# Performance work log

Measured on AMD Instinct MI355X. Metric: run time of the kernel, lower is better.

Reference implementation:

```python
import jax, jax.numpy as jnp
import numpy as np

D_MODEL = 1024
D_INNER = 2048   # expand=2
D_STATE = 16
D_CONV = 4
DT_RANK = 64     # ceil(d_model/16)
B_SZ = 2
L_SEQ = 2048
EPS = 1e-6


def setup_inputs() -> dict:
    key = jax.random.key(0)
    ks = jax.random.split(key, 9)
    def g(k, shape, scale=0.02):
        return jax.random.normal(k, shape, jnp.float32) * scale
    return {
        "x": jax.random.normal(ks[0], (B_SZ, L_SEQ, D_MODEL), jnp.float32),
        "ln_gamma": jnp.ones((D_MODEL,), jnp.float32),
        "ln_beta": jnp.zeros((D_MODEL,), jnp.float32),
        "in_proj_w": g(ks[1], (2 * D_INNER, D_MODEL)),
        "conv_w": g(ks[2], (D_INNER, 1, D_CONV), 0.1),
        "conv_b": g(ks[3], (D_INNER,), 0.1),
        "x_proj_w": g(ks[4], (DT_RANK + 2 * D_STATE, D_INNER)),
        "dt_proj_w": g(ks[5], (D_INNER, DT_RANK), 0.1),
        "dt_proj_b": g(ks[6], (D_INNER,), 0.1),
        "A_log": jnp.log(jnp.broadcast_to(jnp.arange(1, D_STATE + 1, dtype=jnp.float32), (D_INNER, D_STATE))),
        "D": jnp.ones((D_INNER,), jnp.float32),
        "out_proj_w": g(ks[7], (D_MODEL, D_INNER)),
    }


def _silu(v):
    return v * jax.nn.sigmoid(v)


def reference(x, ln_gamma, ln_beta, in_proj_w, conv_w, conv_b, x_proj_w,
              dt_proj_w, dt_proj_b, A_log, D, out_proj_w):
    B, L, _ = x.shape
    # LayerNorm (eps=1e-6)
    mu = x.mean(-1, keepdims=True)
    var = x.var(-1, keepdims=True)
    h = (x - mu) / jnp.sqrt(var + EPS) * ln_gamma + ln_beta
    # in_proj -> (B, 2*d_inner, L)
    xz = jnp.einsum('bld,ed->bel', h, in_proj_w)
    u, z = jnp.split(xz, 2, axis=1)
    # depthwise causal conv1d (padding=d_conv-1, then [..., :L]) + SiLU
    up = jnp.pad(u, ((0, 0), (0, 0), (D_CONV - 1, 0)))
    uc = jax.lax.conv_general_dilated(
        up, conv_w, (1,), 'VALID',
        dimension_numbers=('NCH', 'OIH', 'NCH'),
        feature_group_count=D_INNER)
    uc = _silu(uc + conv_b[None, :, None])  # (B, d_inner, L)
    # x_proj -> dt, B, C
    x_dbl = jnp.einsum('bdl,ed->ble', uc, x_proj_w)
    dt, Bm, Cm = jnp.split(x_dbl, [DT_RANK, DT_RANK + D_STATE], axis=-1)
    delta = jnp.einsum('blr,dr->bdl', dt, dt_proj_w) + dt_proj_b[None, :, None]
    delta = jax.nn.softplus(delta)  # delta_softplus=True with dt_proj bias
    A = -jnp.exp(A_log)  # (d_inner, d_state)
    deltaA = jnp.exp(jnp.einsum('bdl,dn->bdln', delta, A))
    Bm = jnp.transpose(Bm, (0, 2, 1))  # (B, n, L)
    Cm = jnp.transpose(Cm, (0, 2, 1))  # (B, n, L)
    deltaB_u = jnp.einsum('bdl,bnl,bdl->bdln', delta, Bm, uc)

    def step(state, inp):
        dA, dBu, Ct = inp  # (B,d,n), (B,d,n), (B,n)
        state = dA * state + dBu
        y = jnp.einsum('bdn,bn->bd', state, Ct)
        return state, y

    init = jnp.zeros((B, D_INNER, D_STATE), jnp.float32)
    _, ys = jax.lax.scan(
        step, init,
        (jnp.moveaxis(deltaA, 2, 0), jnp.moveaxis(deltaB_u, 2, 0), jnp.moveaxis(Cm, 2, 0)))
    y = jnp.moveaxis(ys, 0, 2)  # (B, d_inner, L)
    y = y + uc * D[None, :, None]
    y = y * _silu(z)
    out = jnp.einsum('bdl,ed->ble', y, out_proj_w)
    return out + x  # residual
```

## Files before the change

kernel.cpp:

```cpp
#include <hip/hip_runtime.h>
#include <hip/hip_bf16.h>

#define D_MODEL 1024
#define D_INNER 2048
#define D_STATE 16
#define D_CONV  4
#define DT_RANK 64
#define B_SZ    2
#define L_SEQ   2048
#define NTOK    (B_SZ * L_SEQ)
#define XD      (DT_RANK + 2 * D_STATE)
#define NCHUNK  64
#define TC      (L_SEQ / NCHUNK)
#define SPLITK  8

#define WS_U     0
#define WS_Z     16777216
#define WS_UC    33554432
#define WS_DY    50331648
#define WS_XDBL  67108864
#define WS_FLAG  67895296
#define WS_NEED  67895552
#define WS_W     67895552
#define OFF_INW  0
#define OFF_OUTW 8388608
#define OFF_XW   12582912
#define OFF_DTW  12976128
#define WS_FULL  81133824

typedef __attribute__((ext_vector_type(8))) short short8;
typedef __attribute__((ext_vector_type(4))) float float4v;

#define GAS __attribute__((address_space(1)))
#define LAS __attribute__((address_space(3)))
__device__ __forceinline__ void gload_lds16(const ushort* g, ushort* l) {
    __builtin_amdgcn_global_load_lds((const GAS uint*)g, (LAS uint*)l, 16, 0, 0);
}

__device__ __forceinline__ float bf2f_u(ushort u) {
    union { uint i; float f; } c; c.i = ((uint)u) << 16; return c.f;
}
__device__ __forceinline__ float u2f(uint u) {
    union { uint i; float f; } c; c.i = u; return c.f;
}
__device__ __forceinline__ ushort f2bf_u(float f) {
    union { float f; uint i; } c; c.f = f;
    uint r = c.i + 0x7FFFu + ((c.i >> 16) & 1u);
    return (ushort)(r >> 16);
}
__device__ __forceinline__ float silu_f(float v) {
    return v * __builtin_amdgcn_rcpf(1.f + __expf(-v));
}
__device__ __forceinline__ float softplus_f(float v) {
    return (v > 15.f) ? v : __logf(1.f + __expf(v));
}
__device__ __forceinline__ int sniff_bf16(const ushort* __restrict__ x) {
    int cnt = 0;
    #pragma unroll
    for (int i = 0; i < 128; i += 2) {
        int e = (x[i] >> 7) & 0xFF;
        cnt += (e >= 120 && e <= 129) ? 1 : 0;
    }
    return cnt >= 32 ? 1 : 0;
}
__device__ __forceinline__ float ldf(const void* p, size_t i, int isbf) {
    return isbf ? bf2f_u(((const ushort*)p)[i]) : ((const float*)p)[i];
}
__device__ __forceinline__ void unpack8(uint4 q, float* v) {
    v[0] = u2f(q.x << 16); v[1] = u2f(q.x & 0xFFFF0000u);
    v[2] = u2f(q.y << 16); v[3] = u2f(q.y & 0xFFFF0000u);
    v[4] = u2f(q.z << 16); v[5] = u2f(q.z & 0xFFFF0000u);
    v[6] = u2f(q.w << 16); v[7] = u2f(q.w & 0xFFFF0000u);
}

__global__ __launch_bounds__(64) void flag_kernel(const ushort* __restrict__ x, int* flag) {
    if (threadIdx.x == 0) *flag = sniff_bf16(x);
}
__global__ __launch_bounds__(256) void ws_marker_kernel(ushort* out, int n, float enc) {
    int i = blockIdx.x * 256 + threadIdx.x;
    if (i < n) out[i] = (i == 0) ? f2bf_u(enc) : (ushort)0;
}
__global__ __launch_bounds__(256) void cvt_kernel(
    const float* __restrict__ src, ushort* __restrict__ dst, int n8)
{
    int i = blockIdx.x * 256 + threadIdx.x;
    if (i >= n8) return;
    const float* s = src + (size_t)i * 8;
    float4 f0 = *(const float4*)s, f1 = *(const float4*)(s + 4);
    ushort o[8];
    o[0] = f2bf_u(f0.x); o[1] = f2bf_u(f0.y); o[2] = f2bf_u(f0.z); o[3] = f2bf_u(f0.w);
    o[4] = f2bf_u(f1.x); o[5] = f2bf_u(f1.y); o[6] = f2bf_u(f1.z); o[7] = f2bf_u(f1.w);
    *(uint4*)(dst + (size_t)i * 8) = *(const uint4*)o;
}

__global__ __launch_bounds__(256) void ln_kernel(
    const void* __restrict__ x, const void* __restrict__ gamma,
    const void* __restrict__ beta, ushort* __restrict__ h,
    const int* __restrict__ wsflag)
{
    int isbf = *wsflag;
    int t = blockIdx.x;
    int tid = threadIdx.x;
    float v[4], s1 = 0.f, s2 = 0.f;
    if (isbf) {
        uint2 raw = *(const uint2*)((const ushort*)x + (size_t)t * D_MODEL + tid * 4);
        const ushort* rs = (const ushort*)&raw;
        #pragma unroll
        for (int i = 0; i < 4; i++) v[i] = bf2f_u(rs[i]);
    } else {
        float4 raw = *(const float4*)((const float*)x + (size_t)t * D_MODEL + tid * 4);
        v[0] = raw.x; v[1] = raw.y; v[2] = raw.z; v[3] = raw.w;
    }
    #pragma unroll
    for (int i = 0; i < 4; i++) { s1 += v[i]; s2 += v[i] * v[i]; }
    #pragma unroll
    for (int off = 32; off; off >>= 1) { s1 += __shfl_down(s1, off); s2 += __shfl_down(s2, off); }
    __shared__ float red1[4], red2[4];
    __shared__ float stats[2];
    int wid = tid >> 6, lane = tid & 63;
    if (lane == 0) { red1[wid] = s1; red2[wid] = s2; }
    __syncthreads();
    if (tid == 0) {
        float a = 0.f, b = 0.f;
        #pragma unroll
        for (int i = 0; i < 4; i++) { a += red1[i]; b += red2[i]; }
        float mu = a * (1.f / D_MODEL);
        float var = b * (1.f / D_MODEL) - mu * mu;
        stats[0] = mu; stats[1] = rsqrtf(var + 1e-6f);
    }
    __syncthreads();
    float mu = stats[0], rstd = stats[1];
    ushort ov[4];
    #pragma unroll
    for (int i = 0; i < 4; i++) {
        float g = ldf(gamma, tid * 4 + i, isbf), bt = ldf(beta, tid * 4 + i, isbf);
        ov[i] = f2bf_u((v[i] - mu) * rstd * g + bt);
    }
    *(uint2*)(h + (size_t)t * D_MODEL + tid * 4) = *(const uint2*)ov;
}

#define TILE_STEP(BC, BS)                                                    \
    do {                                                                     \
        const ushort* ba = &LB[BC][0][0];                                    \
        const ushort* bb = &LB[BC][1][0];                                    \
        short8 av[8]; short8 bv[4];                                          \
        _Pragma("unroll")                                                    \
        for (int mf = 0; mf < 8; mf++)                                       \
            av[mf] = *(const short8*)(ba + offA + mf * 512);                 \
        _Pragma("unroll")                                                    \
        for (int nf = 0; nf < 4; nf++)                                       \
            bv[nf] = *(const short8*)(bb + offB + nf * 512);                 \
        {                                                                    \
            int ko = ((kt + 2) & 31) * 32;                                   \
            ushort* sa = &LB[BS][0][wid * 1024];                             \
            ushort* sb = &LB[BS][1][wid * 1024];                             \
            gload_lds16(gA + ko, sa);                                        \
            gload_lds16(gA + ko + 16 * 1024, sa + 512);                      \
            gload_lds16(gB + ko, sb);                                        \
            gload_lds16(gB + ko + 16 * 1024, sb + 512);                      \
        }                                                                    \
        __builtin_amdgcn_s_setprio(1);                                       \
        _Pragma("unroll")                                                    \
        for (int mf = 0; mf < 8; mf++)                                       \
            _Pragma("unroll")                                                \
            for (int nf = 0; nf < 4; nf++)                                   \
                acc[mf][nf] = __builtin_amdgcn_mfma_f32_16x16x32_bf16(       \
                    av[mf], bv[nf], acc[mf][nf], 0, 0, 0);                   \
        __builtin_amdgcn_s_setprio(0);                                       \
        asm volatile("s_waitcnt vmcnt(4)");                                  \
        __builtin_amdgcn_s_barrier();                                       \
        __builtin_amdgcn_sched_barrier(0);                                   \
        kt++;                                                                \
    } while (0)

__global__ __launch_bounds__(512, 2) void gemm256_inproj(
    const ushort* __restrict__ A,
    const ushort* __restrict__ Bw,
    ushort* __restrict__ U, ushort* __restrict__ Z)
{
    __shared__ __align__(16) ushort LB[3][2][8192];

    int bid = blockIdx.y * 16 + blockIdx.x;
    int xcd = bid & 7, w = bid >> 3;
    int by = (xcd >> 1) * 4 + (w >> 3);
    int bx = (xcd & 1) * 8 + (w & 7);
    int m0 = by * 256, n0 = bx * 256;

    int tid = threadIdx.x;
    int lane = tid & 63, wid = tid >> 6;
    int wm = wid & 1, wn = wid >> 1;
    int lm = lane & 15, quad = lane >> 4;

    int sr = lane >> 2;
    int srow = wid * 32 + sr;
    int sc = ((lane & 3) ^ ((srow >> 1) & 3)) << 3;
    const ushort* gA = A + (size_t)(m0 + srow) * 1024 + sc;
    const ushort* gB = Bw + (size_t)(n0 + srow) * 1024 + sc;

    int posq = (quad ^ ((lm >> 1) & 3)) << 3;
    int offA = (wm * 128 + lm) * 32 + posq;
    int offB = (wn * 64 + lm) * 32 + posq;

    float4v acc[8][4];
    #pragma unroll
    for (int i = 0; i < 8; i++)
        #pragma unroll
        for (int j = 0; j < 4; j++)
            acc[i][j] = (float4v){0.f, 0.f, 0.f, 0.f};

    {
        ushort* sa = &LB[0][0][wid * 1024];
        ushort* sb = &LB[0][1][wid * 1024];
        gload_lds16(gA, sa);
        gload_lds16(gA + 16 * 1024, sa + 512);
        gload_lds16(gB, sb);
        gload_lds16(gB + 16 * 1024, sb + 512);
        sa = &LB[1][0][wid * 1024];
        sb = &LB[1][1][wid * 1024];
        gload_lds16(gA + 32, sa);
        gload_lds16(gA + 32 + 16 * 1024, sa + 512);
        gload_lds16(gB + 32, sb);
        gload_lds16(gB + 32 + 16 * 1024, sb + 512);
    }
    asm volatile("s_waitcnt vmcnt(4)");
    __builtin_amdgcn_s_barrier();
    __builtin_amdgcn_sched_barrier(0);

    int kt = 0;
    #pragma unroll 1
    for (int it = 0; it < 10; it++) {
        TILE_STEP(0, 2);
        TILE_STEP(1, 0);
        TILE_STEP(2, 1);
    }
    TILE_STEP(0, 2);
    TILE_STEP(1, 0);

    __syncthreads();
    ushort* eb = &LB[0][0][0];
    ushort* dst = (n0 < D_INNER) ? U : Z;
    int cn = n0 & (D_INNER - 1);
    int rl = lane >> 3, cl = (lane & 7) * 8;
    #pragma unroll
    for (int pass = 0; pass < 2; pass++) {
        if (pass) __syncthreads();
        if (wm == pass) {
            ushort* ep = eb + wn * (128 * 72);
            #pragma unroll
            for (int mf = 0; mf < 8; mf++)
                #pragma unroll
                for (int nf = 0; nf < 4; nf++)
                    #pragma unroll
                    for (int r = 0; r < 4; r++)
                        ep[(mf * 16 + quad * 4 + r) * 72 + nf * 16 + lm] = f2bf_u(acc[mf][nf][r]);
            #pragma unroll
            for (int itr = 0; itr < 16; itr++) {
                int row = itr * 8 + rl;
                uint4 v = *(const uint4*)(ep + row * 72 + cl);
                *(uint4*)(dst + (size_t)(m0 + pass * 128 + row) * D_INNER + cn + wn * 64 + cl) = v;
            }
        }
    }
}

#define OUT_STEP(BC, BS)                                                     \
    do {                                                                     \
        const ushort* ba = &LB[BC][0];                                       \
        const ushort* bb = &LB[BC][8192];                                    \
        short8 av[8]; short8 bv[2];                                          \
        _Pragma("unroll")                                                    \
        for (int mf = 0; mf < 8; mf++)                                       \
            av[mf] = *(const short8*)(ba + offA + mf * 512);                 \
        _Pragma("unroll")                                                    \
        for (int nf = 0; nf < 2; nf++)                                       \
            bv[nf] = *(const short8*)(bb + offB + nf * 512);                 \
        {                                                                    \
            int ko = ((kt + 2) & 31) * 32;                                   \
            ushort* sa = &LB[BS][wid * 1024];                                \
            ushort* sb = &LB[BS][8192 + wid * 512];                          \
            gload_lds16(gA + ko, sa);                                        \
            gload_lds16(gA + ko + 16 * 2048, sa + 512);                      \
            gload_lds16(gB + ko, sb);                                        \
        }                                                                    \
        __builtin_amdgcn_s_setprio(1);                                       \
        _Pragma("unroll")                                                    \
        for (int mf = 0; mf < 8; mf++)                                       \
            _Pragma("unroll")                                                \
            for (int nf = 0; nf < 2; nf++)                                   \
                acc[mf][nf] = __builtin_amdgcn_mfma_f32_16x16x32_bf16(       \
                    av[mf], bv[nf], acc[mf][nf], 0, 0, 0);                   \
        __builtin_amdgcn_s_setprio(0);                                       \
        asm volatile("s_waitcnt vmcnt(3)");                                  \
        __builtin_amdgcn_s_barrier();                                        \
        __builtin_amdgcn_sched_barrier(0);                                   \
        kt++;                                                                \
    } while (0)

__global__ __launch_bounds__(512, 1) void gemm256_out(
    const ushort* __restrict__ A,
    const ushort* __restrict__ Bw,
    const float* __restrict__ resid,
    float* __restrict__ Cout,
    int kbase)
{
    __shared__ __align__(16) ushort LB[3][12288];

    int bid = blockIdx.y * 8 + blockIdx.x;
    int xcd = bid & 7, w = bid >> 3;
    int by = (xcd & 3) * 4 + (w & 3);
    int bx = (xcd >> 2) * 4 + (w >> 2);
    int m0 = by * 256, n0 = bx * 128;

    int tid = threadIdx.x;
    int lane = tid & 63, wid = tid >> 6;
    int wm = wid & 1, wn = wid >> 1;
    int lm = lane & 15, quad = lane >> 4;

    int sr = lane >> 2;
    int srowA = wid * 32 + sr;
    int scA = ((lane & 3) ^ ((srowA >> 1) & 3)) << 3;
    const ushort* gA = A + (size_t)(m0 + srowA) * 2048 + kbase + scA;
    int srowB = wid * 16 + sr;
    int scB = ((lane & 3) ^ ((srowB >> 1) & 3)) << 3;
    const ushort* gB = Bw + (size_t)(n0 + srowB) * 2048 + kbase + scB;

    int posq = (quad ^ ((lm >> 1) & 3)) << 3;
    int offA = (wm * 128 + lm) * 32 + posq;
    int offB = (wn * 32 + lm) * 32 + posq;

    float4v acc[8][2];
    #pragma unroll
    for (int i = 0; i < 8; i++)
        #pragma unroll
        for (int j = 0; j < 2; j++)
            acc[i][j] = (float4v){0.f, 0.f, 0.f, 0.f};

    {
        ushort* sa = &LB[0][wid * 1024];
        ushort* sb = &LB[0][8192 + wid * 512];
        gload_lds16(gA, sa);
        gload_lds16(gA + 16 * 2048, sa + 512);
        gload_lds16(gB, sb);
        sa = &LB[1][wid * 1024];
        sb = &LB[1][8192 + wid * 512];
        gload_lds16(gA + 32, sa);
        gload_lds16(gA + 32 + 16 * 2048, sa + 512);
        gload_lds16(gB + 32, sb);
    }
    asm volatile("s_waitcnt vmcnt(3)");
    __builtin_amdgcn_s_barrier();
    __builtin_amdgcn_sched_barrier(0);

    int kt = 0;
    #pragma unroll 1
    for (int it = 0; it < 10; it++) {
        OUT_STEP(0, 2);
        OUT_STEP(1, 0);
        OUT_STEP(2, 1);
    }
    OUT_STEP(0, 2);
    OUT_STEP(1, 0);

    __syncthreads();
    float* eb = (float*)&LB[0][0];
    int rl = lane >> 3, cl = (lane & 7) * 4;
    #pragma unroll
    for (int pass = 0; pass < 2; pass++) {
        if (pass) __syncthreads();
        if (wm == pass) {
            float* ep = eb + wn * (128 * 36);
            #pragma unroll
            for (int mf = 0; mf < 8; mf++)
                #pragma unroll
                for (int nf = 0; nf < 2; nf++)
                    #pragma unroll
                    for (int r = 0; r < 4; r++)
                        ep[(mf * 16 + quad * 4 + r) * 36 + nf * 16 + lm] = acc[mf][nf][r];
            #pragma unroll
            for (int itr = 0; itr < 16; itr++) {
                int row = itr * 8 + rl;
                float4 v = *(const float4*)(ep + row * 36 + cl);
                size_t gi = (size_t)(m0 + pass * 128 + row) * D_MODEL + n0 + wn * 32 + cl;
                float4 rv = *(const float4*)(resid + gi);
                v.x += rv.x; v.y += rv.y; v.z += rv.z; v.w += rv.w;
                *(float4*)(Cout + gi) = v;
            }
        }
    }
}

__global__ __launch_bounds__(256) void dt_kernel(
    const ushort* __restrict__ xdbl,
    const ushort* __restrict__ Worig,
    const ushort* __restrict__ Wcvt,
    const void* __restrict__ bias,
    ushort* __restrict__ dy,
    const int* __restrict__ wsflag)
{
    int isbf = *wsflag;
    const ushort* W16 = isbf ? Worig : Wcvt;
    __shared__ __align__(16) ushort EP[4][32 * 64];

    int tid = threadIdx.x, lane = tid & 63, wid = tid >> 6;
    int lm = lane & 15, quad = lane >> 4;
    int t0 = blockIdx.y * 32;
    int d0 = blockIdx.x * 256 + wid * 64;

    short8 a[2][2], b[4][2];
    #pragma unroll
    for (int mf = 0; mf < 2; mf++)
        #pragma unroll
        for (int kk = 0; kk < 2; kk++)
            a[mf][kk] = *(const short8*)(xdbl + (size_t)(t0 + mf * 16 + lm) * XD + kk * 32 + quad * 8);
    #pragma unroll
    for (int nf = 0; nf < 4; nf++)
        #pragma unroll
        for (int kk = 0; kk < 2; kk++)
            b[nf][kk] = *(const short8*)(W16 + (size_t)(d0 + nf * 16 + lm) * 64 + kk * 32 + quad * 8);

    float4v acc[2][4];
    #pragma unroll
    for (int mf = 0; mf < 2; mf++)
        #pragma unroll
        for (int nf = 0; nf < 4; nf++)
            acc[mf][nf] = (float4v){0.f, 0.f, 0.f, 0.f};
    #pragma unroll
    for (int kk = 0; kk < 2; kk++)
        #pragma unroll
        for (int mf = 0; mf < 2; mf++)
            #pragma unroll
            for (int nf = 0; nf < 4; nf++)
                acc[mf][nf] = __builtin_amdgcn_mfma_f32_16x16x32_bf16(
                    a[mf][kk], b[nf][kk], acc[mf][nf], 0, 0, 0);

    float bv[4];
    #pragma unroll
    for (int nf = 0; nf < 4; nf++)
        bv[nf] = ldf(bias, d0 + nf * 16 + lm, isbf);

    ushort* ep = EP[wid];
    #pragma unroll
    for (int mf = 0; mf < 2; mf++)
        #pragma unroll
        for (int nf = 0; nf < 4; nf++)
            #pragma unroll
            for (int r = 0; r < 4; r++)
                ep[(mf * 16 + quad * 4 + r) * 64 + nf * 16 + lm] =
                    f2bf_u(softplus_f(acc[mf][nf][r] + bv[nf]));
    __syncthreads();
    int rl = lane >> 3, cl = (lane & 7) * 8;
    #pragma unroll
    for (int it = 0; it < 4; it++) {
        int row = it * 8 + rl;
        uint4 v = *(const uint4*)(ep + row * 64 + cl);
        *(uint4*)(dy + (size_t)(t0 + row) * D_INNER + d0 + cl) = v;
    }
}

template<int MODE>
__global__ __launch_bounds__(256) void gemm_nt(
    const ushort* __restrict__ A, int lda,
    const void* __restrict__ Bw, const void* __restrict__ Bc, int ldb,
    void* __restrict__ C, int ldc,
    int N, int K,
    const void* __restrict__ bias,
    const void* __restrict__ resid,
    void* __restrict__ C2,
    const int* __restrict__ wsflag)
{
    int isbf = *wsflag;
    const ushort* Bu = (Bc != nullptr && !isbf) ? (const ushort*)Bc : (const ushort*)Bw;
    int bfw = (Bc != nullptr) || isbf;
    __shared__ __align__(16) ushort LB[16384];

    int bx = blockIdx.x, by = blockIdx.y;
    if (MODE == 4) {
        int bid = by * 32 + bx;
        int xcd = bid & 7, w = bid >> 3;
        int pn = w & 7, pm = w >> 3;
        by = (xcd >> 2) * 16 + pm;
        bx = (xcd & 3) * 8 + pn;
    }
    if (MODE == 3) {
        int bid = by * 8 + bx;
        int xcd = bid & 7, w = bid >> 3;
        by = xcd * 4 + (w & 3);
        bx = w >> 2;
    }
    int m0 = by * 128, n0 = bx * 128;
    int kz = (MODE == 5) ? blockIdx.z : 0;
    int kbase = (MODE == 5) ? kz * 256 : 0;

    int tid = threadIdx.x;
    int lane = tid & 63, wid = tid >> 6;
    int wm = wid & 1, wn = wid >> 1;
    int lm = lane & 15, quad = lane >> 4;

    int S0 = wid * 64 + lane;
    int S1 = S0 + 256;
    int r0 = S0 >> 2, r1 = S1 >> 2;
    int cp0 = (S0 & 3) ^ ((S0 >> 3) & 3);
    int cp1 = (S1 & 3) ^ ((S1 >> 3) & 3);
    int ldsOffA0 = (wid * 64) * 8;
    int ldsOffA1 = (256 + wid * 64) * 8;

    const ushort* ga0 = A + (size_t)(m0 + r0) * lda + kbase + cp0 * 8;
    const ushort* ga1 = A + (size_t)(m0 + r1) * lda + kbase + cp1 * 8;
    int nr0 = n0 + r0; if (nr0 > N - 1) nr0 = N - 1;
    int nr1 = n0 + r1; if (nr1 > N - 1) nr1 = N - 1;
    const ushort* gb0 = Bu + (size_t)nr0 * ldb + kbase + cp0 * 8;
    const ushort* gb1 = Bu + (size_t)nr1 * ldb + kbase + cp1 * 8;

    int nk = K >> 5;

    auto issue = [&](int ki) {
        ushort* buf = LB + (ki & 1) * 8192;
        int ko = ki * 32;
        gload_lds16(ga0 + ko, buf + ldsOffA0);
        gload_lds16(ga1 + ko, buf + ldsOffA1);
        if (bfw) {
            gload_lds16(gb0 + ko, buf + 4096 + ldsOffA0);
            gload_lds16(gb1 + ko, buf + 4096 + ldsOffA1);
        } else {
            for (int q = tid; q < 512; q += 256) {
                int S = q, r = S >> 2;
                int cp = (S & 3) ^ ((S >> 3) & 3);
                int nr = n0 + r; if (nr > N - 1) nr = N - 1;
                const float* bp = (const float*)Bw + (size_t)nr * ldb + kbase + ko + cp * 8;
                float4 f0 = *(const float4*)bp, f1 = *(const float4*)(bp + 4);
                ushort tb[8];
                tb[0] = f2bf_u(f0.x); tb[1] = f2bf_u(f0.y); tb[2] = f2bf_u(f0.z); tb[3] = f2bf_u(f0.w);
                tb[4] = f2bf_u(f1.x); tb[5] = f2bf_u(f1.y); tb[6] = f2bf_u(f1.z); tb[7] = f2bf_u(f1.w);
                *(uint4*)(buf + 4096 + (size_t)S * 8) = *(const uint4*)tb;
            }
        }
    };

    float4v acc[4][4];
    #pragma unroll
    for (int i = 0; i < 4; i++)
        #pragma unroll
        for (int j = 0; j < 4; j++)
            acc[i][j] = (float4v){0.f, 0.f, 0.f, 0.f};

    issue(0);
    for (int ki = 0; ki < nk; ki++) {
        __syncthreads();
        if (ki + 1 < nk) issue(ki + 1);
        const ushort* As = LB + (ki & 1) * 8192;
        const ushort* Bs = As + 4096;
        short8 af[4], bfr[4];
        #pragma unroll
        for (int i = 0; i < 4; i++) {
            int r = wm * 64 + i * 16 + lm;
            int cpp = quad ^ ((r >> 1) & 3);
            af[i] = *(const short8*)(As + ((size_t)r * 4 + cpp) * 8);
        }
        #pragma unroll
        for (int j = 0; j < 4; j++) {
            int r = wn * 64 + j * 16 + lm;
            int cpp = quad ^ ((r >> 1) & 3);
            bfr[j] = *(const short8*)(Bs + ((size_t)r * 4 + cpp) * 8);
        }
        #pragma unroll
        for (int i = 0; i < 4; i++)
            #pragma unroll
            for (int j = 0; j < 4; j++)
                acc[i][j] = __builtin_amdgcn_mfma_f32_16x16x32_bf16(af[i], bfr[j], acc[i][j], 0, 0, 0);
    }
    __syncthreads();

    if (MODE == 5) {
        float* Ctf = (float*)LB;
        #pragma unroll
        for (int pass = 0; pass < 2; pass++) {
            if (wm == pass) {
                #pragma unroll
                for (int i = 0; i < 4; i++)
                    #pragma unroll
                    for (int j = 0; j < 4; j++) {
                        int col = wn * 64 + j * 16 + lm;
                        if (col < XD) {
                            #pragma unroll
                            for (int r = 0; r < 4; r++)
                                Ctf[(i * 16 + quad * 4 + r) * 100 + col] = acc[i][j][r];
                        }
                    }
            }
            __syncthreads();
            #pragma unroll
            for (int s = 0; s < 6; s++) {
                int idx = tid + 256 * s;
                int row = idx / 24, q4 = idx - row * 24;
                float4 v = *(const float4*)(Ctf + row * 100 + q4 * 4);
                *(float4*)((float*)C + ((size_t)kz * NTOK + m0 + pass * 64 + row) * XD + q4 * 4) = v;
            }
            __syncthreads();
        }
        return;
    }

    #pragma unroll
    for (int pass = 0; pass < 2; pass++) {
        if (wm == pass) {
            #pragma unroll
            for (int i = 0; i < 4; i++)
                #pragma unroll
                for (int j = 0; j < 4; j++) {
                    int col = wn * 64 + j * 16 + lm;
                    #pragma unroll
                    for (int r = 0; r < 4; r++) {
                        float v = acc[i][j][r];
                        if (MODE == 2) {
                            v += ldf(bias, n0 + col, isbf);
                            v = softplus_f(v);
                        }
                        LB[(size_t)(i * 16 + quad * 4 + r) * 136 + col] = f2bf_u(v);
                    }
                }
        }
        __syncthreads();
        int rb = m0 + pass * 64;
        if (MODE == 3) {
            if (isbf) {
                #pragma unroll
                for (int s = 0; s < 4; s++) {
                    int idx = tid + 256 * s;
                    int row = idx >> 4, q4 = idx & 15;
                    uint4 cv = *(const uint4*)(LB + (size_t)row * 136 + q4 * 8);
                    uint4 rv = *(const uint4*)((const ushort*)resid + (size_t)(rb + row) * ldc + n0 + q4 * 8);
                    float cf[8], rf[8];
                    unpack8(cv, cf); unpack8(rv, rf);
                    ushort o[8];
                    #pragma unroll
                    for (int e = 0; e < 8; e++) o[e] = f2bf_u(cf[e] + rf[e]);
                    *(uint4*)((ushort*)C + (size_t)(rb + row) * ldc + n0 + q4 * 8) = *(const uint4*)o;
                }
            } else {
                #pragma unroll
                for (int s = 0; s < 8; s++) {
                    int idx = tid + 256 * s;
                    int row = idx >> 5, q4 = idx & 31;
                    uint2 cv = *(const uint2*)(LB + (size_t)row * 136 + q4 * 4);
                    float4 rv = *(const float4*)((const float*)resid + (size_t)(rb + row) * ldc + n0 + q4 * 4);
                    float4 o;
                    o.x = u2f(cv.x << 16)          + rv.x;
                    o.y = u2f(cv.x & 0xFFFF0000u)  + rv.y;
                    o.z = u2f(cv.y << 16)          + rv.z;
                    o.w = u2f(cv.y & 0xFFFF0000u)  + rv.w;
                    *(float4*)((float*)C + (size_t)(rb + row) * ldc + n0 + q4 * 4) = o;
                }
            }
        } else {
            ushort* dst; int colb, ldd;
            if (MODE == 4) {
                dst = (n0 < D_INNER) ? (ushort*)C : (ushort*)C2;
                colb = n0 & (D_INNER - 1); ldd = D_INNER;
            } else {
                dst = (ushort*)C; colb = n0; ldd = ldc;
            }
            #pragma unroll
            for (int s = 0; s < 4; s++) {
                int idx = tid + 256 * s;
                int row = idx >> 4, q4 = idx & 15;
                uint4 cv = *(const uint4*)(LB + (size_t)row * 136 + q4 * 8);
                *(uint4*)(dst + (size_t)(rb + row) * ldd + colb + q4 * 8) = cv;
            }
        }
        __syncthreads();
    }
}

__global__ __launch_bounds__(256) void xproj_reduce(
    const float* __restrict__ part, ushort* __restrict__ xdbl)
{
    int i = blockIdx.x * 256 + threadIdx.x;
    float s = 0.f;
    #pragma unroll
    for (int kz = 0; kz < SPLITK; kz++)
        s += part[(size_t)kz * (NTOK * XD) + i];
    xdbl[i] = f2bf_u(s);
}

__global__ __launch_bounds__(256) void conv_silu_kernel(
    const ushort* __restrict__ u, const void* __restrict__ cw,
    const void* __restrict__ cb, ushort* __restrict__ uc,
    const int* __restrict__ wsflag)
{
    int isbf = *wsflag;
    int t = blockIdx.x;
    int d8 = threadIdx.x * 8;
    int l = t & (L_SEQ - 1);

    float wv[32];
    if (isbf) {
        const ushort* p = (const ushort*)cw + (size_t)d8 * 4;
        unpack8(*(const uint4*)p,        wv);
        unpack8(*(const uint4*)(p + 8),  wv + 8);
        unpack8(*(const uint4*)(p + 16), wv + 16);
        unpack8(*(const uint4*)(p + 24), wv + 24);
    } else {
        const float* p = (const float*)cw + (size_t)d8 * 4;
        #pragma unroll
        for (int i = 0; i < 8; i++) {
            float4 f = *(const float4*)(p + i * 4);
            wv[i * 4 + 0] = f.x; wv[i * 4 + 1] = f.y;
            wv[i * 4 + 2] = f.z; wv[i * 4 + 3] = f.w;
        }
    }
    float bv[8];
    if (isbf) {
        unpack8(*(const uint4*)((const ushort*)cb + d8), bv);
    } else {
        const float* p = (const float*)cb + d8;
        float4 f0 = *(const float4*)p, f1 = *(const float4*)(p + 4);
        bv[0] = f0.x; bv[1] = f0.y; bv[2] = f0.z; bv[3] = f0.w;
        bv[4] = f1.x; bv[5] = f1.y; bv[6] = f1.z; bv[7] = f1.w;
    }

    float ur[4][8];
    #pragma unroll
    for (int k = 0; k < 4; k++) {
        int lp = l - 3 + k;
        if (lp >= 0) {
            unpack8(*(const uint4*)(u + (size_t)(t - 3 + k) * D_INNER + d8), ur[k]);
        } else {
            #pragma unroll
            for (int j = 0; j < 8; j++) ur[k][j] = 0.f;
        }
    }

    ushort o[8];
    #pragma unroll
    for (int j = 0; j < 8; j++) {
        float acc = bv[j];
        #pragma unroll
        for (int k = 0; k < 4; k++)
            acc += ur[k][j] * wv[j * 4 + k];
        o[j] = f2bf_u(silu_f(acc));
    }
    *(uint4*)(uc + (size_t)t * D_INNER + d8) = *(const uint4*)o;
}

__global__ __launch_bounds__(256) void scan_phase1(
    const ushort* __restrict__ delta, const ushort* __restrict__ uc,
    const ushort* __restrict__ xdbl,
    ushort* __restrict__ aprod, ushort* __restrict__ spart)
{
    int b = blockIdx.z, c = blockIdx.y;
    int d = blockIdx.x * 256 + threadIdx.x;
    float st[16];
    #pragma unroll
    for (int n = 0; n < 16; n++) st[n] = 0.f;
    float P = 1.f;
    int t0 = b * L_SEQ + c * TC;
    for (int i = 0; i < TC; ++i) {
        int t = t0 + i;
        float dlt = bf2f_u(delta[(size_t)t * 2048 + d]);
        float uv  = bf2f_u(uc[(size_t)t * 2048 + d]);
        float Bv[16];
        unpack8(*(const uint4*)(xdbl + (size_t)t * XD + DT_RANK), Bv);
        unpack8(*(const uint4*)(xdbl + (size_t)t * XD + DT_RANK + 8), Bv + 8);
        float du = dlt * uv;
        float E = __expf(-dlt);
        P *= E;
        float E2 = E * E, E4 = E2 * E2, E8 = E4 * E4;
        float c1 = E, c2 = E2, c3 = E * E2, c4 = E4;
        float c5 = E4 * E, c6 = E4 * E2, c7 = E4 * c3, c8 = E8;
        float c9 = E8 * E, c10 = E8 * E2, c11 = E8 * c3, c12 = E8 * E4;
        float c13 = E8 * c5, c14 = E8 * c6, c15 = E8 * c7, c16 = E8 * E8;
        st[0]  = c1  * st[0]  + du * Bv[0];
        st[1]  = c2  * st[1]  + du * Bv[1];
        st[2]  = c3  * st[2]  + du * Bv[2];
        st[3]  = c4  * st[3]  + du * Bv[3];
        st[4]  = c5  * st[4]  + du * Bv[4];
        st[5]  = c6  * st[5]  + du * Bv[5];
        st[6]  = c7  * st[6]  + du * Bv[6];
        st[7]  = c8  * st[7]  + du * Bv[7];
        st[8]  = c9  * st[8]  + du * Bv[8];
        st[9]  = c10 * st[9]  + du * Bv[9];
        st[10] = c11 * st[10] + du * Bv[10];
        st[11] = c12 * st[11] + du * Bv[11];
        st[12] = c13 * st[12] + du * Bv[12];
        st[13] = c14 * st[13] + du * Bv[13];
        st[14] = c15 * st[14] + du * Bv[14];
        st[15] = c16 * st[15] + du * Bv[15];
    }
    size_t base = ((size_t)((b * NCHUNK + c) * D_INNER + d)) * 16;
    ushort apb[16], stb[16];
    {
        float P2 = P * P, P4 = P2 * P2, P8 = P4 * P4;
        float q1 = P, q2 = P2, q3 = P * P2, q4 = P4;
        float q5 = P4 * P, q6 = P4 * P2, q7 = P4 * q3, q8 = P8;
        float q9 = P8 * P, q10 = P8 * P2, q11 = P8 * q3, q12 = P8 * P4;
        float q13 = P8 * q5, q14 = P8 * q6, q15 = P8 * q7, q16 = P8 * P8;
        apb[0] = f2bf_u(q1);  apb[1] = f2bf_u(q2);  apb[2] = f2bf_u(q3);  apb[3] = f2bf_u(q4);
        apb[4] = f2bf_u(q5);  apb[5] = f2bf_u(q6);  apb[6] = f2bf_u(q7);  apb[7] = f2bf_u(q8);
        apb[8] = f2bf_u(q9);  apb[9] = f2bf_u(q10); apb[10] = f2bf_u(q11); apb[11] = f2bf_u(q12);
        apb[12] = f2bf_u(q13); apb[13] = f2bf_u(q14); apb[14] = f2bf_u(q15); apb[15] = f2bf_u(q16);
    }
    #pragma unroll
    for (int n = 0; n < 16; n++) stb[n] = f2bf_u(st[n]);
    *(uint4*)(aprod + base)     = *(const uint4*)apb;
    *(uint4*)(aprod + base + 8) = *(const uint4*)(apb + 8);
    *(uint4*)(spart + base)     = *(const uint4*)stb;
    *(uint4*)(spart + base + 8) = *(const uint4*)(stb + 8);
}

__global__ __launch_bounds__(256) void scan_phase2(
    const ushort* __restrict__ aprod, ushort* __restrict__ spart)
{
    size_t i = (size_t)blockIdx.x * 256 + threadIdx.x;
    int b = (int)(i >> 15);
    size_t r = i & 32767;
    float s = 0.f;
    for (int c = 0; c < NCHUNK; ++c) {
        size_t idx = ((size_t)(b * NCHUNK + c) << 15) + r;
        float init = s;
        s = bf2f_u(aprod[idx]) * s + bf2f_u(spart[idx]);
        spart[idx] = f2bf_u(init);
    }
}

__global__ __launch_bounds__(256) void scan_phase3(
    ushort* dy, const ushort* __restrict__ uc,
    const ushort* __restrict__ xdbl, const ushort* __restrict__ z,
    const void* __restrict__ Dp, const ushort* __restrict__ spart,
    const int* __restrict__ wsflag)
{
    int isbf = *wsflag;
    int b = blockIdx.z, c = blockIdx.y;
    int d = blockIdx.x * 256 + threadIdx.x;
    float st[16];
    size_t base = ((size_t)((b * NCHUNK + c) * D_INNER + d)) * 16;
    unpack8(*(const uint4*)(spart + base), st);
    unpack8(*(const uint4*)(spart + base + 8), st + 8);
    float Dv = ldf(Dp, d, isbf);
    int t0 = b * L_SEQ + c * TC;
    for (int i = 0; i < TC; ++i) {
        int t = t0 + i;
        float dlt = bf2f_u(dy[(size_t)t * 2048 + d]);
        float uv  = bf2f_u(uc[(size_t)t * 2048 + d]);
        float Bv[16], Cv[16];
        unpack8(*(const uint4*)(xdbl + (size_t)t * XD + DT_RANK), Bv);
        unpack8(*(const uint4*)(xdbl + (size_t)t * XD + DT_RANK + 8), Bv + 8);
        unpack8(*(const uint4*)(xdbl + (size_t)t * XD + DT_RANK + 16), Cv);
        unpack8(*(const uint4*)(xdbl + (size_t)t * XD + DT_RANK + 24), Cv + 8);
        float du = dlt * uv;
        float E = __expf(-dlt);
        float E2 = E * E, E4 = E2 * E2, E8 = E4 * E4;
        float c1 = E, c2 = E2, c3 = E * E2, c4 = E4;
        float c5 = E4 * E, c6 = E4 * E2, c7 = E4 * c3, c8 = E8;
        float c9 = E8 * E, c10 = E8 * E2, c11 = E8 * c3, c12 = E8 * E4;
        float c13 = E8 * c5, c14 = E8 * c6, c15 = E8 * c7, c16 = E8 * E8;
        float p = 0.f;
        st[0]  = c1  * st[0]  + du * Bv[0];  p += st[0]  * Cv[0];
        st[1]  = c2  * st[1]  + du * Bv[1];  p += st[1]  * Cv[1];
        st[2]  = c3  * st[2]  + du * Bv[2];  p += st[2]  * Cv[2];
        st[3]  = c4  * st[3]  + du * Bv[3];  p += st[3]  * Cv[3];
        st[4]  = c5  * st[4]  + du * Bv[4];  p += st[4]  * Cv[4];
        st[5]  = c6  * st[5]  + du * Bv[5];  p += st[5]  * Cv[5];
        st[6]  = c7  * st[6]  + du * Bv[6];  p += st[6]  * Cv[6];
        st[7]  = c8  * st[7]  + du * Bv[7];  p += st[7]  * Cv[7];
        st[8]  = c9  * st[8]  + du * Bv[8];  p += st[8]  * Cv[8];
        st[9]  = c10 * st[9]  + du * Bv[9];  p += st[9]  * Cv[9];
        st[10] = c11 * st[10] + du * Bv[10]; p += st[10] * Cv[10];
        st[11] = c12 * st[11] + du * Bv[11]; p += st[11] * Cv[11];
        st[12] = c13 * st[12] + du * Bv[12]; p += st[12] * Cv[12];
        st[13] = c14 * st[13] + du * Bv[13]; p += st[13] * Cv[13];
        st[14] = c15 * st[14] + du * Bv[14]; p += st[14] * Cv[14];
        st[15] = c16 * st[15] + du * Bv[15]; p += st[15] * Cv[15];
        float zv = bf2f_u(z[(size_t)t * 2048 + d]);
        dy[(size_t)t * 2048 + d] = f2bf_u((p + uv * Dv) * silu_f(zv));
    }
}

extern "C" void kernel_launch(void* const* d_in, const int* in_sizes, int n_in,
                              void* d_out, int out_size, void* d_ws, size_t ws_size,
                              hipStream_t stream) {
    const void* x         = d_in[0];
    const void* ln_gamma  = d_in[1];
    const void* ln_beta   = d_in[2];
    const void* in_proj_w = d_in[3];
    const void* conv_w    = d_in[4];
    const void* conv_b    = d_in[5];
    const void* x_proj_w  = d_in[6];
    const void* dt_proj_w = d_in[7];
    const void* dt_proj_b = d_in[8];
    const void* Dp        = d_in[10];
    const void* out_proj_w= d_in[11];
    const ushort* xraw    = (const ushort*)d_in[0];

    if (ws_size < (size_t)WS_NEED) {
        float enc = 1000.f + (float)(ws_size >> 20);
        ws_marker_kernel<<<(out_size + 255) / 256, 256, 0, stream>>>((ushort*)d_out, out_size, enc);
        return;
    }
    const bool haveW = ws_size >= (size_t)WS_FULL;

    char* ws = (char*)d_ws;
    ushort* u      = (ushort*)(ws + WS_U);
    ushort* z      = (ushort*)(ws + WS_Z);
    ushort* uc     = (ushort*)(ws + WS_UC);
    ushort* dy     = (ushort*)(ws + WS_DY);
    ushort* xdbl   = (ushort*)(ws + WS_XDBL);
    int*    wsflag = (int*)(ws + WS_FLAG);
    float*  xpart  = (float*)(ws + WS_U);
    ushort* aprod  = (ushort*)(ws + WS_U);
    ushort* spart  = (ushort*)(ws + WS_U + 8388608);
    ushort* w_in   = haveW ? (ushort*)(ws + WS_W + OFF_INW)  : nullptr;
    ushort* w_out  = haveW ? (ushort*)(ws + WS_W + OFF_OUTW) : nullptr;
    ushort* w_x    = haveW ? (ushort*)(ws + WS_W + OFF_XW)   : nullptr;
    ushort* w_dt   = haveW ? (ushort*)(ws + WS_W + OFF_DTW)  : nullptr;

    flag_kernel<<<1, 64, 0, stream>>>(xraw, wsflag);

    if (haveW) {
        cvt_kernel<<<(4194304/8 + 255)/256, 256, 0, stream>>>((const float*)in_proj_w,  w_in,  4194304/8);
        cvt_kernel<<<(2097152/8 + 255)/256, 256, 0, stream>>>((const float*)out_proj_w, w_out, 2097152/8);
        cvt_kernel<<<( 196608/8 + 255)/256, 256, 0, stream>>>((const float*)x_proj_w,   w_x,    196608/8);
        cvt_kernel<<<( 131072/8 + 255)/256, 256, 0, stream>>>((const float*)dt_proj_w,  w_dt,   131072/8);
    }

    ln_kernel<<<NTOK, 256, 0, stream>>>(x, ln_gamma, ln_beta, dy, wsflag);

    if (haveW) {
        gemm256_inproj<<<dim3(16, 16), 512, 0, stream>>>(dy, w_in, u, z);
    } else {
        gemm_nt<4><<<dim3(32, 32), 256, 0, stream>>>(
            dy, D_MODEL, in_proj_w, w_in, D_MODEL, u, D_INNER,
            2 * D_INNER, D_MODEL, nullptr, nullptr, z, wsflag);
    }

    conv_silu_kernel<<<NTOK, 256, 0, stream>>>(u, conv_w, conv_b, uc, wsflag);

    gemm_nt<5><<<dim3(1, 32, SPLITK), 256, 0, stream>>>(
        uc, D_INNER, x_proj_w, w_x, D_INNER, xpart, XD,
        XD, D_INNER / SPLITK, nullptr, nullptr, nullptr, wsflag);
    xproj_reduce<<<(NTOK * XD) / 256, 256, 0, stream>>>(xpart, xdbl);

    if (haveW) {
        dt_kernel<<<dim3(8, 128), 256, 0, stream>>>(
            xdbl, (const ushort*)dt_proj_w, w_dt, dt_proj_b, dy, wsflag);
    } else {
        gemm_nt<2><<<dim3(16, 32), 256, 0, stream>>>(
            xdbl, XD, dt_proj_w, w_dt, DT_RANK, dy, D_INNER,
            D_INNER, DT_RANK, dt_proj_b, nullptr, nullptr, wsflag);
    }

    scan_phase1<<<dim3(D_INNER / 256, NCHUNK, B_SZ), 256, 0, stream>>>(
        dy, uc, xdbl, aprod, spart);
    scan_phase2<<<(B_SZ * D_INNER * D_STATE) / 256, 256, 0, stream>>>(aprod, spart);
    scan_phase3<<<dim3(D_INNER / 256, NCHUNK, B_SZ), 256, 0, stream>>>(
        dy, uc, xdbl, z, Dp, spart, wsflag);

    if (haveW) {
        gemm256_out<<<dim3(8, 16), 512, 0, stream>>>(
            dy, w_out, (const float*)x, (float*)d_out, 0);
        gemm256_out<<<dim3(8, 16), 512, 0, stream>>>(
            dy, w_out, (const float*)d_out, (float*)d_out, 1024);
    } else {
        gemm_nt<3><<<dim3(8, 32), 256, 0, stream>>>(
            dy, D_INNER, out_proj_w, w_out, D_INNER, d_out, D_MODEL,
            D_MODEL, D_INNER, nullptr, x, nullptr, wsflag);
    }
}
```

Baseline: 299.2 us.

## Fuse weight conversions with flag sniff and retile out_proj GEMM to single full-K pass

The four fp32-to-bf16 weight conversion launches and the flag-sniff launch are merged into one kernel, which cuts launch overhead. The out_proj GEMM moves from two split-K launches on 256x128 tiles to one full-K launch on 128x128 tiles with 256 blocks and two blocks per CU. This removes the second pass that re-read and re-wrote the fp32 output and gives better CU occupancy. In exchange each tile does less reuse per block and runs a longer K loop.

Measured after the change: 283.3 us. 1.06x faster.

```diff
diff --git a/kernel.cpp b/kernel.cpp
--- a/kernel.cpp
+++ b/kernel.cpp
@@ -80,17 +80,32 @@
     int i = blockIdx.x * 256 + threadIdx.x;
     if (i < n) out[i] = (i == 0) ? f2bf_u(enc) : (ushort)0;
 }
-__global__ __launch_bounds__(256) void cvt_kernel(
-    const float* __restrict__ src, ushort* __restrict__ dst, int n8)
+
+#define N8_INW  524288
+#define N8_OUTW 262144
+#define N8_XW   24576
+#define N8_DTW  16384
+#define N8_TOT  (N8_INW + N8_OUTW + N8_XW + N8_DTW)
+__global__ __launch_bounds__(256) void cvt_all_kernel(
+    const float* __restrict__ inw, const float* __restrict__ outw,
+    const float* __restrict__ xw, const float* __restrict__ dtw,
+    ushort* __restrict__ w_in, ushort* __restrict__ w_out,
+    ushort* __restrict__ w_x, ushort* __restrict__ w_dt,
+    const ushort* __restrict__ xraw, int* flag)
 {
     int i = blockIdx.x * 256 + threadIdx.x;
-    if (i >= n8) return;
-    const float* s = src + (size_t)i * 8;
+    if (blockIdx.x == 0 && threadIdx.x == 0) *flag = sniff_bf16(xraw);
+    const float* src; ushort* dst; int j;
+    if (i < N8_INW)                     { src = inw;  dst = w_in;  j = i; }
+    else if (i < N8_INW + N8_OUTW)      { src = outw; dst = w_out; j = i - N8_INW; }
+    else if (i < N8_INW + N8_OUTW + N8_XW) { src = xw; dst = w_x;  j = i - N8_INW - N8_OUTW; }
+    else                                { src = dtw;  dst = w_dt;  j = i - N8_INW - N8_OUTW - N8_XW; }
+    const float* s = src + (size_t)j * 8;
     float4 f0 = *(const float4*)s, f1 = *(const float4*)(s + 4);
     ushort o[8];
     o[0] = f2bf_u(f0.x); o[1] = f2bf_u(f0.y); o[2] = f2bf_u(f0.z); o[3] = f2bf_u(f0.w);
     o[4] = f2bf_u(f1.x); o[5] = f2bf_u(f1.y); o[6] = f2bf_u(f1.z); o[7] = f2bf_u(f1.w);
-    *(uint4*)(dst + (size_t)i * 8) = *(const uint4*)o;
+    *(uint4*)(dst + (size_t)j * 8) = *(const uint4*)o;
 }
 
 __global__ __launch_bounds__(256) void ln_kernel(
@@ -168,7 +183,7 @@
                     av[mf], bv[nf], acc[mf][nf], 0, 0, 0);                   \
         __builtin_amdgcn_s_setprio(0);                                       \
         asm volatile("s_waitcnt vmcnt(4)");                                  \
-        __builtin_amdgcn_s_barrier();                                       \
+        __builtin_amdgcn_s_barrier();                                        \
         __builtin_amdgcn_sched_barrier(0);                                   \
         kt++;                                                                \
     } while (0)
@@ -263,128 +278,112 @@
     }
 }
 
-#define OUT_STEP(BC, BS)                                                     \
+#define OUT2_STEP(BC, BS)                                                    \
     do {                                                                     \
         const ushort* ba = &LB[BC][0];                                       \
-        const ushort* bb = &LB[BC][8192];                                    \
-        short8 av[8]; short8 bv[2];                                          \
+        const ushort* bb = &LB[BC][4096];                                    \
+        short8 av[4]; short8 bv[2];                                          \
         _Pragma("unroll")                                                    \
-        for (int mf = 0; mf < 8; mf++)                                       \
+        for (int mf = 0; mf < 4; mf++)                                       \
             av[mf] = *(const short8*)(ba + offA + mf * 512);                 \
         _Pragma("unroll")                                                    \
         for (int nf = 0; nf < 2; nf++)                                       \
             bv[nf] = *(const short8*)(bb + offB + nf * 512);                 \
         {                                                                    \
-            int ko = ((kt + 2) & 31) * 32;                                   \
-            ushort* sa = &LB[BS][wid * 1024];                                \
-            ushort* sb = &LB[BS][8192 + wid * 512];                          \
-            gload_lds16(gA + ko, sa);                                        \
-            gload_lds16(gA + ko + 16 * 2048, sa + 512);                      \
-            gload_lds16(gB + ko, sb);                                        \
+            int ko = ((kt + 2) & 63) * 32;                                   \
+            gload_lds16(gA + ko, &LB[BS][wid * 512]);                        \
+            gload_lds16(gB + ko, &LB[BS][4096 + wid * 512]);                 \
         }                                                                    \
         __builtin_amdgcn_s_setprio(1);                                       \
         _Pragma("unroll")                                                    \
-        for (int mf = 0; mf < 8; mf++)                                       \
+        for (int mf = 0; mf < 4; mf++)                                       \
             _Pragma("unroll")                                                \
             for (int nf = 0; nf < 2; nf++)                                   \
                 acc[mf][nf] = __builtin_amdgcn_mfma_f32_16x16x32_bf16(       \
                     av[mf], bv[nf], acc[mf][nf], 0, 0, 0);                   \
         __builtin_amdgcn_s_setprio(0);                                       \
-        asm volatile("s_waitcnt vmcnt(3)");                                  \
+        asm volatile("s_waitcnt vmcnt(2)");                                  \
         __builtin_amdgcn_s_barrier();                                        \
         __builtin_amdgcn_sched_barrier(0);                                   \
         kt++;                                                                \
     } while (0)
 
-__global__ __launch_bounds__(512, 1) void gemm256_out(
+__global__ __launch_bounds__(512, 2) void gemm256_out2(
     const ushort* __restrict__ A,
     const ushort* __restrict__ Bw,
     const float* __restrict__ resid,
-    float* __restrict__ Cout,
-    int kbase)
-{
-    __shared__ __align__(16) ushort LB[3][12288];
+    float* __restrict__ Cout)
+{
+    __shared__ __align__(16) ushort LB[3][8192];
 
     int bid = blockIdx.y * 8 + blockIdx.x;
     int xcd = bid & 7, w = bid >> 3;
-    int by = (xcd & 3) * 4 + (w & 3);
-    int bx = (xcd >> 2) * 4 + (w >> 2);
-    int m0 = by * 256, n0 = bx * 128;
+    int by = xcd * 4 + (w & 3);
+    int bx = w >> 2;
+    int m0 = by * 128, n0 = bx * 128;
 
     int tid = threadIdx.x;
     int lane = tid & 63, wid = tid >> 6;
     int wm = wid & 1, wn = wid >> 1;
     int lm = lane & 15, quad = lane >> 4;
 
-    int sr = lane >> 2;
-    int srowA = wid * 32 + sr;
-    int scA = ((lane & 3) ^ ((srowA >> 1) & 3)) << 3;
-    const ushort* gA = A + (size_t)(m0 + srowA) * 2048 + kbase + scA;
-    int srowB = wid * 16 + sr;
-    int scB = ((lane & 3) ^ ((srowB >> 1) & 3)) << 3;
-    const ushort* gB = Bw + (size_t)(n0 + srowB) * 2048 + kbase + scB;
+    int srow = tid >> 2;
+    int sc = ((tid & 3) ^ ((srow >> 1) & 3)) << 3;
+    const ushort* gA = A + (size_t)(m0 + srow) * 2048 + sc;
+    const ushort* gB = Bw + (size_t)(n0 + srow) * 2048 + sc;
 
     int posq = (quad ^ ((lm >> 1) & 3)) << 3;
-    int offA = (wm * 128 + lm) * 32 + posq;
+    int offA = (wm * 64 + lm) * 32 + posq;
     int offB = (wn * 32 + lm) * 32 + posq;
 
-    float4v acc[8][2];
-    #pragma unroll
-    for (int i = 0; i < 8; i++)
+    float4v acc[4][2];
+    #pragma unroll
+    for (int i = 0; i < 4; i++)
         #pragma unroll
         for (int j = 0; j < 2; j++)
             acc[i][j] = (float4v){0.f, 0.f, 0.f, 0.f};
 
-    {
-        ushort* sa = &LB[0][wid * 1024];
-        ushort* sb = &LB[0][8192 + wid * 512];
-        gload_lds16(gA, sa);
-        gload_lds16(gA + 16 * 2048, sa + 512);
-        gload_lds16(gB, sb);
-        sa = &LB[1][wid * 1024];
-        sb = &LB[1][8192 + wid * 512];
-        gload_lds16(gA + 32, sa);
-        gload_lds16(gA + 32 + 16 * 2048, sa + 512);
-        gload_lds16(gB + 32, sb);
-    }
-    asm volatile("s_waitcnt vmcnt(3)");
+    gload_lds16(gA, &LB[0][wid * 512]);
+    gload_lds16(gB, &LB[0][4096 + wid * 512]);
+    gload_lds16(gA + 32, &LB[1][wid * 512]);
+    gload_lds16(gB + 32, &LB[1][4096 + wid * 512]);
+    asm volatile("s_waitcnt vmcnt(2)");
     __builtin_amdgcn_s_barrier();
     __builtin_amdgcn_sched_barrier(0);
 
     int kt = 0;
     #pragma unroll 1
-    for (int it = 0; it < 10; it++) {
-        OUT_STEP(0, 2);
-        OUT_STEP(1, 0);
-        OUT_STEP(2, 1);
-    }
-    OUT_STEP(0, 2);
-    OUT_STEP(1, 0);
+    for (int it = 0; it < 21; it++) {
+        OUT2_STEP(0, 2);
+        OUT2_STEP(1, 0);
+        OUT2_STEP(2, 1);
+    }
+    OUT2_STEP(0, 2);
 
     __syncthreads();
     float* eb = (float*)&LB[0][0];
-    int rl = lane >> 3, cl = (lane & 7) * 4;
     #pragma unroll
     for (int pass = 0; pass < 2; pass++) {
         if (pass) __syncthreads();
         if (wm == pass) {
-            float* ep = eb + wn * (128 * 36);
             #pragma unroll
-            for (int mf = 0; mf < 8; mf++)
+            for (int mf = 0; mf < 4; mf++)
                 #pragma unroll
                 for (int nf = 0; nf < 2; nf++)
                     #pragma unroll
                     for (int r = 0; r < 4; r++)
-                        ep[(mf * 16 + quad * 4 + r) * 36 + nf * 16 + lm] = acc[mf][nf][r];
-            #pragma unroll
-            for (int itr = 0; itr < 16; itr++) {
-                int row = itr * 8 + rl;
-                float4 v = *(const float4*)(ep + row * 36 + cl);
-                size_t gi = (size_t)(m0 + pass * 128 + row) * D_MODEL + n0 + wn * 32 + cl;
-                float4 rv = *(const float4*)(resid + gi);
-                v.x += rv.x; v.y += rv.y; v.z += rv.z; v.w += rv.w;
-                *(float4*)(Cout + gi) = v;
-            }
+                        eb[(mf * 16 + quad * 4 + r) * 132 + wn * 32 + nf * 16 + lm] = acc[mf][nf][r];
+        }
+        __syncthreads();
+        #pragma unroll
+        for (int s = 0; s < 4; s++) {
+            int idx = tid + 512 * s;
+            int row = idx >> 5, c4 = (idx & 31) * 4;
+            float4 v = *(const float4*)(eb + row * 132 + c4);
+            size_t gi = (size_t)(m0 + pass * 64 + row) * D_MODEL + n0 + c4;
+            float4 rv = *(const float4*)(resid + gi);
+            v.x += rv.x; v.y += rv.y; v.z += rv.z; v.w += rv.w;
+            *(float4*)(Cout + gi) = v;
         }
     }
 }
@@ -913,13 +912,13 @@
     ushort* w_x    = haveW ? (ushort*)(ws + WS_W + OFF_XW)   : nullptr;
     ushort* w_dt   = haveW ? (ushort*)(ws + WS_W + OFF_DTW)  : nullptr;
 
-    flag_kernel<<<1, 64, 0, stream>>>(xraw, wsflag);
-
     if (haveW) {
-        cvt_kernel<<<(4194304/8 + 255)/256, 256, 0, stream>>>((const float*)in_proj_w,  w_in,  4194304/8);
-        cvt_kernel<<<(2097152/8 + 255)/256, 256, 0, stream>>>((const float*)out_proj_w, w_out, 2097152/8);
-        cvt_kernel<<<( 196608/8 + 255)/256, 256, 0, stream>>>((const float*)x_proj_w,   w_x,    196608/8);
-        cvt_kernel<<<( 131072/8 + 255)/256, 256, 0, stream>>>((const float*)dt_proj_w,  w_dt,   131072/8);
+        cvt_all_kernel<<<N8_TOT / 256, 256, 0, stream>>>(
+            (const float*)in_proj_w, (const float*)out_proj_w,
+            (const float*)x_proj_w, (const float*)dt_proj_w,
+            w_in, w_out, w_x, w_dt, xraw, wsflag);
+    } else {
+        flag_kernel<<<1, 64, 0, stream>>>(xraw, wsflag);
     }
 
     ln_kernel<<<NTOK, 256, 0, stream>>>(x, ln_gamma, ln_beta, dy, wsflag);
@@ -955,10 +954,8 @@
         dy, uc, xdbl, z, Dp, spart, wsflag);
 
     if (haveW) {
-        gemm256_out<<<dim3(8, 16), 512, 0, stream>>>(
-            dy, w_out, (const float*)x, (float*)d_out, 0);
-        gemm256_out<<<dim3(8, 16), 512, 0, stream>>>(
-            dy, w_out, (const float*)d_out, (float*)d_out, 1024);
+        gemm256_out2<<<dim3(8, 32), 512, 0, stream>>>(
+            dy, w_out, (const float*)x, (float*)d_out);
     } else {
         gemm_nt<3><<<dim3(8, 32), 256, 0, stream>>>(
             dy, D_INNER, out_proj_w, w_out, D_INNER, d_out, D_MODEL,
```
